# Kernel tuning notes

Measured on AMD Instinct MI355X. Metric: run time of the kernel, lower is better.

## Reference

```python
import jax, jax.numpy as jnp
import numpy as np

B, T, P, D, V = 8, 4096, 4, 512, 256
N = T // P          # 1024 patches (T divisible by P, so no padding needed)
K = 16              # k_retrieval
W = 4               # local message-passing window
H = 8               # refresh attention heads = min(8, D//64)
ROUNDS = 6
EPS = 1e-5


def layer_norm(x, g, b):
    mu = x.mean(-1, keepdims=True)
    var = ((x - mu) ** 2).mean(-1, keepdims=True)
    return (x - mu) / jnp.sqrt(var + EPS) * g + b


def setup_inputs() -> dict:
    key = jax.random.key(0)
    ks = iter(jax.random.split(key, 48))
    w = lambda *s: jax.random.normal(next(ks), s, jnp.float32) * 0.02
    p = {}
    p['x'] = jax.random.randint(next(ks), (B, T), 0, V)
    p['emb'] = w(V, D)
    p['pos_emb'] = w(P, D)
    p['gru_w_ih'] = w(D, 3 * D); p['gru_w_hh'] = w(D, 3 * D)
    p['gru_b_ih'] = jnp.zeros(3 * D); p['gru_b_hh'] = jnp.zeros(3 * D)
    p['patch_ln_g'] = jnp.ones(D); p['patch_ln_b'] = jnp.zeros(D)
    p['summ_w'] = w(D, D); p['summ_b'] = jnp.zeros(D)
    p['msg_w1'] = w(2 * D, D); p['msg_b1'] = jnp.zeros(D)
    p['msg_w2'] = w(D, D); p['msg_b2'] = jnp.zeros(D)
    p['msg_ln_g'] = jnp.ones(D); p['msg_ln_b'] = jnp.zeros(D)
    p['q_w'] = w(D, D); p['q_b'] = jnp.zeros(D)
    p['k_w'] = w(D, D); p['k_b'] = jnp.zeros(D)
    p['v_w'] = w(D, D); p['v_b'] = jnp.zeros(D)
    p['o_w'] = w(D, D); p['o_b'] = jnp.zeros(D)
    p['gc_w_ih'] = w(2 * D, 3 * D); p['gc_w_hh'] = w(D, 3 * D)
    p['gc_b_ih'] = jnp.zeros(3 * D); p['gc_b_hh'] = jnp.zeros(3 * D)
    p['ar_ln_g'] = jnp.ones(D); p['ar_ln_b'] = jnp.zeros(D)
    p['ar_qkv_w'] = w(D, 3 * D); p['ar_qkv_b'] = jnp.zeros(3 * D)
    p['ar_out_w'] = w(D, D); p['ar_out_b'] = jnp.zeros(D)
    p['broad_w'] = w(D, D); p['broad_b'] = jnp.zeros(D)
    p['ln_g'] = jnp.ones(D); p['ln_b'] = jnp.zeros(D)
    p['head_w'] = w(D, V)
    return p


def reference(x, emb, pos_emb, gru_w_ih, gru_w_hh, gru_b_ih, gru_b_hh,
              patch_ln_g, patch_ln_b, summ_w, summ_b,
              msg_w1, msg_b1, msg_w2, msg_b2, msg_ln_g, msg_ln_b,
              q_w, q_b, k_w, k_b, v_w, v_b, o_w, o_b,
              gc_w_ih, gc_w_hh, gc_b_ih, gc_b_hh,
              ar_ln_g, ar_ln_b, ar_qkv_w, ar_qkv_b, ar_out_w, ar_out_b,
              broad_w, broad_b, ln_g, ln_b, head_w):
    # --- patch encoding: embedding + pos + GRU over the P tokens of each patch ---
    flat = x.reshape(B * N, P)
    h = emb[flat] + pos_emb[None, :, :]                      # [B*N, P, D]

    def gru_step(hprev, xt):
        gi = xt @ gru_w_ih + gru_b_ih
        gh = hprev @ gru_w_hh + gru_b_hh
        ir, iz, inn = jnp.split(gi, 3, -1)
        hr, hz, hn = jnp.split(gh, 3, -1)
        r = jax.nn.sigmoid(ir + hr)
        z = jax.nn.sigmoid(iz + hz)
        n = jnp.tanh(inn + r * hn)
        hnew = (1 - z) * n + z * hprev
        return hnew, hnew

    _, hs = jax.lax.scan(gru_step, jnp.zeros((B * N, D), h.dtype), jnp.swapaxes(h, 0, 1))
    local = layer_norm(jnp.swapaxes(hs, 0, 1), patch_ln_g, patch_ln_b).reshape(B, N, P, D)
    h = local.mean(2) @ summ_w + summ_b                      # patch summaries [B, N, D]

    # --- RoPE tables over patch positions ---
    d = D // 2
    inv_freq = 1.0 / (10000.0 ** (jnp.arange(0, D, 2, dtype=jnp.float32) / D))
    freqs = jnp.arange(N, dtype=jnp.float32)[:, None] * inv_freq[None, :]   # [N, d]
    cos, sin = jnp.cos(freqs), jnp.sin(freqs)

    def rotary(t):
        t1, t2 = t[..., :d], t[..., d:]
        return jnp.concatenate([t1 * cos - t2 * sin, t2 * cos + t1 * sin], -1)

    causal = jnp.tril(jnp.ones((N, N), bool))
    hd = D // H

    for rnd in range(ROUNDS):
        # windowed neighbor gather (W past patches + self), fused MLP messages
        padded = jnp.pad(h, ((0, 0), (W, 0), (0, 0)))
        neighbors = jnp.stack([padded[:, W - w:W - w + N] for w in range(W + 1)], 2)  # [B,N,W+1,D]
        self_exp = jnp.broadcast_to(h[:, :, None, :], neighbors.shape)
        msg_in = jnp.concatenate([self_exp, neighbors], -1)
        msgs = (jax.nn.gelu(msg_in @ msg_w1 + msg_b1, approximate=False) @ msg_w2 + msg_b2).mean(2)

        # RoPE top-k sparse causal attention (N > K, sparse branch always taken)
        q = rotary(h @ q_w + q_b)
        k = rotary(h @ k_w + k_b)
        v = h @ v_w + v_b
        scores = jnp.einsum('bnd,bmd->bnm', q, k) / jnp.sqrt(jnp.float32(D))
        scores = jnp.where(causal, scores, -jnp.inf)
        tv, ti = jax.lax.top_k(scores, K)
        probs = jax.nn.softmax(tv, -1)  # == softmax of -inf-filled sparse score matrix
        vg = jax.vmap(lambda vi, ii: vi[ii])(v, ti)          # [B, N, K, D]
        retrieved = jnp.einsum('bnk,bnkd->bnd', probs, vg) @ o_w + o_b

        # GRUCell gated write
        wi = jnp.concatenate([msgs, retrieved], -1)
        gi = wi @ gc_w_ih + gc_b_ih
        gh = h @ gc_w_hh + gc_b_hh
        ir, iz, inn = jnp.split(gi, 3, -1)
        hr, hz, hn = jnp.split(gh, 3, -1)
        r = jax.nn.sigmoid(ir + hr)
        z = jax.nn.sigmoid(iz + hz)
        n = jnp.tanh(inn + r * hn)
        h = layer_norm((1 - z) * n + z * h, msg_ln_g, msg_ln_b)

        # global causal MHA refresh every 2 rounds (eval mode, no dropout)
        if (rnd + 1) % 2 == 0:
            res = h
            hn_ = layer_norm(h, ar_ln_g, ar_ln_b)
            qkv = hn_ @ ar_qkv_w + ar_qkv_b
            qh, kh, vh = [t.reshape(B, N, H, hd) for t in jnp.split(qkv, 3, -1)]
            s = jnp.einsum('bnhd,bmhd->bhnm', qh, kh) / jnp.sqrt(jnp.float32(hd))
            a = jax.nn.softmax(jnp.where(causal, s, -jnp.inf), -1)
            o = jnp.einsum('bhnm,bmhd->bnhd', a, vh).reshape(B, N, D)
            h = res + (o @ ar_out_w + ar_out_b)

    # broadcast patch state back to tokens, project to vocab
    broad = h @ broad_w + broad_b
    final = (local + broad[:, :, None, :]).reshape(B, N * P, D)[:, :T]
    return layer_norm(final, ln_g, ln_b) @ head_w            # [B, T, V]
```

## Files before the change

kernel.cpp:

```cpp
#include <hip/hip_runtime.h>
#include <math.h>

constexpr int CB = 8, CT = 4096, CP = 4, CD = 512, CV = 256;
constexpr int CN = 1024, CK = 16, CH = 8, CHD = 64;
constexpr int ROWS = CB * CN;
constexpr int TROWS = CB * CT;
constexpr float CEPS = 1e-5f;
constexpr size_t PN = (size_t)ROWS * CD;

constexpr size_t OFF_LOCAL = 0;
constexpr size_t OFF_HP    = OFF_LOCAL + (size_t)ROWS * CP * CD;
constexpr size_t OFF_X4    = OFF_HP    + PN;
constexpr size_t OFF_MS    = OFF_X4    + (size_t)ROWS * 2560;
constexpr size_t OFF_A     = OFF_MS    + PN;
constexpr size_t OFF_B     = OFF_A     + PN;
constexpr size_t OFF_BIAS  = OFF_B     + PN;
constexpr size_t OFF_WT    = OFF_BIAS  + 4096;

constexpr size_t TOT_W    = 7471104;
constexpr size_t T_GRU_IH = 0;
constexpr size_t T_GRU_HH = 786432;
constexpr size_t T_SUMM   = 1572864;
constexpr size_t T_FUSE   = 1835008;
constexpr size_t T_MSG2   = 3145728;
constexpr size_t T_OW     = 3407872;
constexpr size_t T_GCAB   = 3670016;
constexpr size_t T_GC_HH  = 5242880;
constexpr size_t T_AR_QKV = 6029312;
constexpr size_t T_AR_OUT = 6815744;
constexpr size_t T_BROAD  = 7077888;
constexpr size_t T_HEAD   = 7340032;

constexpr int F_ACC_F32  = 1;
constexpr int F_ACC_PAIR = 2;
constexpr int F_WR_F32   = 4;
constexpr int F_WR_PAIR  = 8;
constexpr int F_TRI      = 16;
constexpr int F_SPLIT    = 32;

typedef __attribute__((ext_vector_type(8))) short short8;
typedef __attribute__((ext_vector_type(4))) float f32x4;

__device__ __forceinline__ float sigm(float x) { return 1.f / (1.f + expf(-x)); }
__device__ __forceinline__ float geluf(float x) {
  return 0.5f * x * (1.f + erff(x * 0.7071067811865475f));
}
__device__ __forceinline__ unsigned short bf_hi(float x) {
  const unsigned u = __float_as_uint(x);
  return (unsigned short)((u + 0x7FFFu + ((u >> 16) & 1u)) >> 16);
}
__device__ __forceinline__ float bf_f(unsigned short h) {
  return __uint_as_float((unsigned)h << 16);
}
__device__ __forceinline__ void split_store(float v, unsigned short* ph, unsigned short* pl) {
  const unsigned short h = bf_hi(v);
  *ph = h; *pl = bf_hi(v - bf_f(h));
}
__device__ __forceinline__ float blk_sum(float v, float* red) {
#pragma unroll
  for (int o = 32; o > 0; o >>= 1) v += __shfl_down(v, o, 64);
  const int wv = threadIdx.x >> 6, ln = threadIdx.x & 63;
  __syncthreads();
  if (ln == 0) red[wv] = v;
  __syncthreads();
  return red[0] + red[1] + red[2] + red[3];
}

__global__ __launch_bounds__(256) void transpose_split(const float* __restrict__ in,
                                                       unsigned short* __restrict__ oh,
                                                       unsigned short* __restrict__ ol,
                                                       int K, int N, int ldk, int ko)
{
  __shared__ float tile[32][33];
  const int n0 = blockIdx.x * 32, k0 = blockIdx.y * 32;
  const int tx = threadIdx.x & 31, ty = threadIdx.x >> 5;
#pragma unroll
  for (int i = 0; i < 32; i += 8)
    tile[ty + i][tx] = in[(size_t)(k0 + ty + i) * N + n0 + tx];
  __syncthreads();
#pragma unroll
  for (int i = 0; i < 32; i += 8) {
    const float v = tile[tx][ty + i];
    const unsigned short h = bf_hi(v);
    const size_t o = (size_t)(n0 + ty + i) * ldk + ko + k0 + tx;
    oh[o] = h;
    ol[o] = bf_hi(v - bf_f(h));
  }
}

__global__ void concat_bias5(const float* __restrict__ b1, const float* __restrict__ qb,
                             const float* __restrict__ kb, const float* __restrict__ vb,
                             float* __restrict__ o)
{
  const int i = blockIdx.x * 256 + threadIdx.x;
  float v;
  if (i < 512) v = b1[i];
  else if (i < 1024) v = 0.f;
  else if (i < 1536) v = qb[i - 1024];
  else if (i < 2048) v = kb[i - 1536];
  else v = vb[i - 2048];
  o[i] = v;
}

template <bool P3>
__global__ __launch_bounds__(256, 2) void gemm_bf3(
    const unsigned short* __restrict__ AH, const unsigned short* __restrict__ AL,
    const unsigned short* __restrict__ A2H, const unsigned short* __restrict__ A2L,
    int K1, int lda,
    const unsigned short* __restrict__ BH, const unsigned short* __restrict__ BL, int ldb,
    const float* __restrict__ bias, float scale,
    float* __restrict__ Cf, int ldc, float* __restrict__ Cf2,
    unsigned short* __restrict__ CHp, unsigned short* __restrict__ CLp, int ldcp,
    int K, int flags, long long sA, long long sB, long long sC)
{
  AH += (size_t)blockIdx.z * sA; AL += (size_t)blockIdx.z * sA;
  BH += (size_t)blockIdx.z * sB; BL += (size_t)blockIdx.z * sB;
  if (Cf) Cf += (size_t)blockIdx.z * sC;
  int bm, bn;
  if (flags & F_TRI) {
    int t = blockIdx.x, i = 0, acc = 0;
    while (acc + i + 1 <= t) { ++i; acc += i; }
    bm = i << 7; bn = (t - acc) << 7;
  } else {
    bm = blockIdx.y << 7; bn = blockIdx.x << 7;
  }
  __shared__ __align__(16) unsigned short AsH[128][40];
  __shared__ __align__(16) unsigned short AsL[128][40];
  __shared__ __align__(16) unsigned short BsH[128][40];
  __shared__ __align__(16) unsigned short BsL[P3 ? 128 : 1][40];
  const int tid = threadIdx.x;
  const int lane = tid & 63, wave = tid >> 6;
  const int wm = (wave & 1) << 6, wn = (wave >> 1) << 6;
  const int r16 = lane & 15, quad = lane >> 4;
  const int sr = tid >> 1, sc = (tid & 1) << 4;
  const f32x4 zero = {0.f, 0.f, 0.f, 0.f};
  f32x4 acc[4][4];
#pragma unroll
  for (int i = 0; i < 4; ++i)
#pragma unroll
    for (int j = 0; j < 4; ++j) acc[i][j] = zero;

  for (int k0 = 0; k0 < K; k0 += 32) {
    const int kc = k0 + sc;
    const unsigned short *pAH, *pAL;
    if (kc < K1) {
      pAH = AH + (size_t)(bm + sr) * lda + kc;
      pAL = AL + (size_t)(bm + sr) * lda + kc;
    } else {
      pAH = A2H + (size_t)(bm + sr) * lda + (kc - K1);
      pAL = A2L + (size_t)(bm + sr) * lda + (kc - K1);
    }
    const unsigned short* pBH = BH + (size_t)(bn + sr) * ldb + kc;
    *(uint4*)&AsH[sr][sc]     = *(const uint4*)pAH;
    *(uint4*)&AsH[sr][sc + 8] = *(const uint4*)(pAH + 8);
    *(uint4*)&AsL[sr][sc]     = *(const uint4*)pAL;
    *(uint4*)&AsL[sr][sc + 8] = *(const uint4*)(pAL + 8);
    *(uint4*)&BsH[sr][sc]     = *(const uint4*)pBH;
    *(uint4*)&BsH[sr][sc + 8] = *(const uint4*)(pBH + 8);
    if (P3) {
      const unsigned short* pBL = BL + (size_t)(bn + sr) * ldb + kc;
      *(uint4*)&BsL[sr][sc]     = *(const uint4*)pBL;
      *(uint4*)&BsL[sr][sc + 8] = *(const uint4*)(pBL + 8);
    }
    __syncthreads();
    short8 bh[4], bl[4];
#pragma unroll
    for (int ni = 0; ni < 4; ++ni) {
      bh[ni] = *(const short8*)&BsH[wn + ni * 16 + r16][quad * 8];
      if (P3) bl[ni] = *(const short8*)&BsL[wn + ni * 16 + r16][quad * 8];
    }
#pragma unroll
    for (int mi = 0; mi < 4; ++mi) {
      const short8 ah = *(const short8*)&AsH[wm + mi * 16 + r16][quad * 8];
      const short8 al = *(const short8*)&AsL[wm + mi * 16 + r16][quad * 8];
#pragma unroll
      for (int ni = 0; ni < 4; ++ni) {
        acc[mi][ni] = __builtin_amdgcn_mfma_f32_16x16x32_bf16(ah, bh[ni], acc[mi][ni], 0, 0, 0);
        acc[mi][ni] = __builtin_amdgcn_mfma_f32_16x16x32_bf16(al, bh[ni], acc[mi][ni], 0, 0, 0);
        if (P3)
          acc[mi][ni] = __builtin_amdgcn_mfma_f32_16x16x32_bf16(ah, bl[ni], acc[mi][ni], 0, 0, 0);
      }
    }
    __syncthreads();
  }
#pragma unroll
  for (int mi = 0; mi < 4; ++mi) {
    const int row0 = bm + wm + mi * 16 + quad * 4;
#pragma unroll
    for (int ni = 0; ni < 4; ++ni) {
      const int col = bn + wn + ni * 16 + r16;
      const float bv = bias ? bias[col] : 0.f;
#pragma unroll
      for (int rg = 0; rg < 4; ++rg) {
        const int row = row0 + rg;
        float o = acc[mi][ni][rg] * scale + bv;
        if (flags & F_SPLIT) {
          if (col < 1024) {
            float* p = Cf + (size_t)row * ldc + col;
            *p = o + *p;
          } else {
            Cf2[(size_t)row * 512 + (col - 1024)] = o;
          }
        } else {
          if (flags & F_ACC_F32) o += Cf[(size_t)row * ldc + col];
          if (flags & F_ACC_PAIR) {
            const size_t ip = (size_t)row * ldcp + col;
            o += bf_f(CHp[ip]) + bf_f(CLp[ip]);
          }
          if (flags & F_WR_F32) Cf[(size_t)row * ldc + col] = o;
          if (flags & F_WR_PAIR) {
            const size_t ip = (size_t)row * ldcp + col;
            split_store(o, &CHp[ip], &CLp[ip]);
          }
        }
      }
    }
  }
}

__global__ __launch_bounds__(256, 3) void gemm_bf3s(
    const unsigned short* __restrict__ AH, const unsigned short* __restrict__ AL, int lda,
    const unsigned short* __restrict__ BH, int ldb,
    const float* __restrict__ bias,
    float* __restrict__ Cf, int ldc,
    unsigned short* __restrict__ CHp, unsigned short* __restrict__ CLp, int ldcp,
    int K, int flags)
{
  const int bm = blockIdx.y << 6, bn = blockIdx.x << 7;
  __shared__ __align__(16) unsigned short AsH[64][40];
  __shared__ __align__(16) unsigned short AsL[64][40];
  __shared__ __align__(16) unsigned short BsH[128][40];
  const int tid = threadIdx.x;
  const int lane = tid & 63, wave = tid >> 6;
  const int wm = (wave & 1) << 5, wn = (wave >> 1) << 6;
  const int r16 = lane & 15, quad = lane >> 4;
  const int sar = tid >> 2, sac = (tid & 3) << 3;
  const int sbr = tid >> 1, sbc = (tid & 1) << 4;
  const f32x4 zero = {0.f, 0.f, 0.f, 0.f};
  f32x4 acc[2][4];
#pragma unroll
  for (int i = 0; i < 2; ++i)
#pragma unroll
    for (int j = 0; j < 4; ++j) acc[i][j] = zero;

  for (int k0 = 0; k0 < K; k0 += 32) {
    const unsigned short* pAH = AH + (size_t)(bm + sar) * lda + k0 + sac;
    const unsigned short* pAL = AL + (size_t)(bm + sar) * lda + k0 + sac;
    const unsigned short* pBH = BH + (size_t)(bn + sbr) * ldb + k0 + sbc;
    *(uint4*)&AsH[sar][sac] = *(const uint4*)pAH;
    *(uint4*)&AsL[sar][sac] = *(const uint4*)pAL;
    *(uint4*)&BsH[sbr][sbc]     = *(const uint4*)pBH;
    *(uint4*)&BsH[sbr][sbc + 8] = *(const uint4*)(pBH + 8);
    __syncthreads();
    short8 bh[4];
#pragma unroll
    for (int ni = 0; ni < 4; ++ni)
      bh[ni] = *(const short8*)&BsH[wn + ni * 16 + r16][quad * 8];
#pragma unroll
    for (int mi = 0; mi < 2; ++mi) {
      const short8 ah = *(const short8*)&AsH[wm + mi * 16 + r16][quad * 8];
      const short8 al = *(const short8*)&AsL[wm + mi * 16 + r16][quad * 8];
#pragma unroll
      for (int ni = 0; ni < 4; ++ni) {
        acc[mi][ni] = __builtin_amdgcn_mfma_f32_16x16x32_bf16(ah, bh[ni], acc[mi][ni], 0, 0, 0);
        acc[mi][ni] = __builtin_amdgcn_mfma_f32_16x16x32_bf16(al, bh[ni], acc[mi][ni], 0, 0, 0);
      }
    }
    __syncthreads();
  }
#pragma unroll
  for (int mi = 0; mi < 2; ++mi) {
    const int row0 = bm + wm + mi * 16 + quad * 4;
#pragma unroll
    for (int ni = 0; ni < 4; ++ni) {
      const int col = bn + wn + ni * 16 + r16;
      const float bv = bias ? bias[col] : 0.f;
#pragma unroll
      for (int rg = 0; rg < 4; ++rg) {
        const int row = row0 + rg;
        float o = acc[mi][ni][rg] + bv;
        if (flags & F_ACC_PAIR) {
          const size_t ip = (size_t)row * ldcp + col;
          o += bf_f(CHp[ip]) + bf_f(CLp[ip]);
        }
        if (flags & F_WR_F32) Cf[(size_t)row * ldc + col] = o;
        if (flags & F_WR_PAIR) {
          const size_t ip = (size_t)row * ldcp + col;
          split_store(o, &CHp[ip], &CLp[ip]);
        }
      }
    }
  }
}

__global__ void zero_k(float* __restrict__ p) {
  p[(size_t)blockIdx.x * 256 + threadIdx.x] = 0.f;
}

__global__ void embed_p(const int* __restrict__ x, const float* __restrict__ emb,
                        const float* __restrict__ pos,
                        unsigned short* __restrict__ oh, unsigned short* __restrict__ ol, int t)
{
  const int i = blockIdx.x * 256 + threadIdx.x;
  const int r = i >> 9, d = i & 511;
  const int b = r >> 10, n = r & (CN - 1);
  const int tok = x[b * CT + n * CP + t];
  const float v = emb[(size_t)tok * CD + d] + pos[t * CD + d];
  split_store(v, &oh[i], &ol[i]);
}

__global__ void gru_point_p(const float* __restrict__ gi, const float* __restrict__ ghn,
                            unsigned short* __restrict__ hH, unsigned short* __restrict__ hL,
                            float* __restrict__ hs, int t)
{
  const int i = blockIdx.x * 256 + threadIdx.x;
  const int r = i >> 9, d = i & 511;
  const size_t gb = (size_t)r * (3 * CD) + d;
  const float sr_ = gi[gb], sz = gi[gb + CD], inn = gi[gb + 2 * CD];
  const float hn = ghn[i];
  const float hp = bf_f(hH[i]) + bf_f(hL[i]);
  const float rr = sigm(sr_), zz = sigm(sz);
  const float nn = tanhf(inn + rr * hn);
  const float hv = (1.f - zz) * nn + zz * hp;
  split_store(hv, &hH[i], &hL[i]);
  hs[(size_t)r * (CP * CD) + (size_t)t * CD + d] = hv;
}

__global__ __launch_bounds__(256) void ln_rows(const float* __restrict__ in, float* __restrict__ out,
                                               const float* __restrict__ g, const float* __restrict__ b)
{
  const int r = blockIdx.x, t = threadIdx.x;
  __shared__ float red[4];
  const float* ip = in + (size_t)r * CD;
  const float v0 = ip[t], v1 = ip[t + 256];
  const float mu = blk_sum(v0 + v1, red) * (1.f / CD);
  const float d0 = v0 - mu, d1 = v1 - mu;
  const float var = blk_sum(d0 * d0 + d1 * d1, red) * (1.f / CD);
  const float inv = rsqrtf(var + CEPS);
  float* op = out + (size_t)r * CD;
  op[t] = d0 * inv * g[t] + b[t];
  op[t + 256] = d1 * inv * g[t + 256] + b[t + 256];
}

__global__ void mean_pool_p(const float* __restrict__ local,
                            unsigned short* __restrict__ oh, unsigned short* __restrict__ ol)
{
  const int i = blockIdx.x * 256 + threadIdx.x;
  const int r = i >> 9, d = i & 511;
  const float* p = local + (size_t)r * (CP * CD) + d;
  split_store(0.25f * (p[0] + p[CD] + p[2 * CD] + p[3 * CD]), &oh[i], &ol[i]);
}

__global__ void msg_gelu_p(const float* __restrict__ X4,
                           unsigned short* __restrict__ oh, unsigned short* __restrict__ ol)
{
  const int i = blockIdx.x * 256 + threadIdx.x;
  const int r = i >> 9, d = i & 511;
  const int n = r & (CN - 1);
  const float pv = X4[(size_t)r * 2560 + d];
  float acc = 0.f;
#pragma unroll
  for (int w = 0; w <= 4; ++w) {
    const float xv = pv + ((n >= w) ? X4[(size_t)(r - w) * 2560 + 512 + d] : 0.f);
    acc += geluf(xv);
  }
  split_store(acc * 0.2f, &oh[i], &ol[i]);
}

__global__ void rotary2_p(const float* __restrict__ X4,
                          unsigned short* __restrict__ qh, unsigned short* __restrict__ ql,
                          unsigned short* __restrict__ kh, unsigned short* __restrict__ kl)
{
  const int i = blockIdx.x * 256 + threadIdx.x;
  const int r = i >> 8, j = i & 255;
  const int n = r & (CN - 1);
  const float fr = (float)n * expf(-9.210340371976184f * ((float)j * (1.f / 256.f)));
  float s, c;
  sincosf(fr, &s, &c);
  const float* p = X4 + (size_t)r * 2560;
  const size_t o0 = (size_t)r * CD + j, o1 = o0 + 256;
  const float q1 = p[1024 + j], q2 = p[1024 + 256 + j];
  split_store(q1 * c - q2 * s, &qh[o0], &ql[o0]);
  split_store(q2 * c + q1 * s, &qh[o1], &ql[o1]);
  const float k1 = p[1536 + j], k2 = p[1536 + 256 + j];
  split_store(k1 * c - k2 * s, &kh[o0], &kl[o0]);
  split_store(k2 * c + k1 * s, &kh[o1], &kl[o1]);
}

__global__ __launch_bounds__(256) void topk_attn(const float* __restrict__ X4,
                                                 unsigned short* __restrict__ ctxH,
                                                 unsigned short* __restrict__ ctxL)
{
  const int r = blockIdx.x;
  const int b = r >> 10, n = r & (CN - 1);
  const float* row = X4 + (size_t)r * 2560;
  const int tid = threadIdx.x, lane = tid & 63, wave = tid >> 6;
  __shared__ unsigned long long cands[64];
  __shared__ float p16[CK];
  __shared__ int i16[CK];
  unsigned long long key[4];
#pragma unroll
  for (int q = 0; q < 4; ++q) {
    const int m = tid + q * 256;
    const float v = (m <= n) ? row[m] : -INFINITY;
    unsigned u = __float_as_uint(v);
    u = (u & 0x80000000u) ? ~u : (u | 0x80000000u);
    key[q] = ((unsigned long long)u << 32) | (unsigned)(CN - 1 - m);
  }
  unsigned long long mycand = 0ull;
#pragma unroll
  for (int it = 0; it < CK; ++it) {
    unsigned long long best = key[0];
#pragma unroll
    for (int q = 1; q < 4; ++q) best = best > key[q] ? best : key[q];
#pragma unroll
    for (int o = 32; o > 0; o >>= 1) {
      const unsigned long long o2 = __shfl_xor(best, o, 64);
      best = best > o2 ? best : o2;
    }
    if (lane == it) mycand = best;
#pragma unroll
    for (int q = 0; q < 4; ++q)
      if (key[q] == best) key[q] = 0ull;
  }
  if (lane < CK) cands[wave * CK + lane] = mycand;
  __syncthreads();
  if (wave == 0) {
    unsigned long long k2 = cands[lane];
    unsigned long long mine = 0ull;
#pragma unroll
    for (int it = 0; it < CK; ++it) {
      unsigned long long best = k2;
#pragma unroll
      for (int o = 32; o > 0; o >>= 1) {
        const unsigned long long o2 = __shfl_xor(best, o, 64);
        best = best > o2 ? best : o2;
      }
      if (lane == it) mine = best;
      if (k2 == best) k2 = 0ull;
    }
    unsigned u = (unsigned)(mine >> 32);
    u = (u & 0x80000000u) ? (u & 0x7FFFFFFFu) : ~u;
    const float val = __uint_as_float(u);
    const int idx = CN - 1 - (int)(mine & 0xFFFFFFFFu);
    const float mx = __shfl(val, 0, 64);
    float e = 0.f;
    if (lane < CK && val != -INFINITY) e = expf(val - mx);
    float sum = e;
#pragma unroll
    for (int o = 32; o > 0; o >>= 1) sum += __shfl_xor(sum, o, 64);
    if (lane < CK) {
      p16[lane] = e / sum;
      i16[lane] = idx;
    }
  }
  __syncthreads();
  const size_t vb = ((size_t)b << 10);
#pragma unroll
  for (int pass = 0; pass < 2; ++pass) {
    const int d = tid + pass * 256;
    float a = 0.f;
#pragma unroll
    for (int q = 0; q < CK; ++q)
      a += p16[q] * X4[(vb + i16[q]) * 2560 + 2048 + d];
    split_store(a, &ctxH[(size_t)r * CD + d], &ctxL[(size_t)r * CD + d]);
  }
}

__global__ __launch_bounds__(256) void gru_ln_p(const float* __restrict__ gi, const float* __restrict__ ghn,
                                                unsigned short* __restrict__ hH, unsigned short* __restrict__ hL,
                                                const float* __restrict__ g, const float* __restrict__ b,
                                                unsigned short* __restrict__ aH, unsigned short* __restrict__ aL,
                                                const float* __restrict__ g2, const float* __restrict__ b2)
{
  const int r = blockIdx.x, t = threadIdx.x;
  __shared__ float red[4];
  float u[2];
#pragma unroll
  for (int q = 0; q < 2; ++q) {
    const int d = t + q * 256;
    const size_t gb = (size_t)r * (3 * CD) + d;
    const float sr_ = gi[gb], sz = gi[gb + CD], inn = gi[gb + 2 * CD];
    const float hn = ghn[(size_t)r * CD + d];
    const size_t hi = (size_t)r * CD + d;
    const float hp = bf_f(hH[hi]) + bf_f(hL[hi]);
    const float rr = sigm(sr_), zz = sigm(sz);
    const float nn = tanhf(inn + rr * hn);
    u[q] = (1.f - zz) * nn + zz * hp;
  }
  const float mu = blk_sum(u[0] + u[1], red) * (1.f / CD);
  const float d0 = u[0] - mu, d1 = u[1] - mu;
  const float var = blk_sum(d0 * d0 + d1 * d1, red) * (1.f / CD);
  const float inv = rsqrtf(var + CEPS);
  const float h0 = d0 * inv * g[t] + b[t];
  const float h1 = d1 * inv * g[t + 256] + b[t + 256];
  split_store(h0, &hH[(size_t)r * CD + t], &hL[(size_t)r * CD + t]);
  split_store(h1, &hH[(size_t)r * CD + t + 256], &hL[(size_t)r * CD + t + 256]);
  if (aH) {
    const float mu2 = blk_sum(h0 + h1, red) * (1.f / CD);
    const float e0 = h0 - mu2, e1 = h1 - mu2;
    const float var2 = blk_sum(e0 * e0 + e1 * e1, red) * (1.f / CD);
    const float inv2 = rsqrtf(var2 + CEPS);
    split_store(e0 * inv2 * g2[t] + b2[t], &aH[(size_t)r * CD + t], &aL[(size_t)r * CD + t]);
    split_store(e1 * inv2 * g2[t + 256] + b2[t + 256],
                &aH[(size_t)r * CD + t + 256], &aL[(size_t)r * CD + t + 256]);
  }
}

constexpr int FP = 72;
__global__ __launch_bounds__(256, 2) void flash_attn_p(const unsigned short* __restrict__ qkvH,
                                                       const unsigned short* __restrict__ qkvL,
                                                       unsigned short* __restrict__ outH,
                                                       unsigned short* __restrict__ outL)
{
  __shared__ __align__(16) unsigned short Qh[64 * FP], Ql[64 * FP];
  __shared__ __align__(16) unsigned short Kh[64 * FP], Kl[64 * FP];
  __shared__ __align__(16) unsigned short Vth[64 * FP], Vtl[64 * FP];
  __shared__ __align__(16) unsigned short Pm[64 * FP];
  const int qt = blockIdx.x, head = blockIdx.y, b = blockIdx.z;
  const int tid = threadIdx.x;
  const int lane = tid & 63, wave = tid >> 6;
  const int r16 = lane & 15, quad = lane >> 4;
  const size_t base = (size_t)b * CN * (3 * CD) + head * CHD;

  {
    const int r = tid >> 2, c0 = (tid & 3) << 4;
    const unsigned short* qh = qkvH + base + (size_t)(qt * 64 + r) * (3 * CD) + c0;
    const unsigned short* ql = qkvL + base + (size_t)(qt * 64 + r) * (3 * CD) + c0;
    *(uint4*)&Qh[r * FP + c0]     = *(const uint4*)qh;
    *(uint4*)&Qh[r * FP + c0 + 8] = *(const uint4*)(qh + 8);
    *(uint4*)&Ql[r * FP + c0]     = *(const uint4*)ql;
    *(uint4*)&Ql[r * FP + c0 + 8] = *(const uint4*)(ql + 8);
  }
  float m_i[4], l_i[4];
  f32x4 O[4];
  const f32x4 zero = {0.f, 0.f, 0.f, 0.f};
#pragma unroll
  for (int r = 0; r < 4; ++r) { m_i[r] = -INFINITY; l_i[r] = 0.f; }
#pragma unroll
  for (int d = 0; d < 4; ++d) O[d] = zero;

  for (int j = 0; j <= qt; ++j) {
    __syncthreads();
    {
      const int r = tid >> 2, c0 = (tid & 3) << 4;
      const unsigned short* kh = qkvH + base + (size_t)(j * 64 + r) * (3 * CD) + CD + c0;
      const unsigned short* kl = qkvL + base + (size_t)(j * 64 + r) * (3 * CD) + CD + c0;
      *(uint4*)&Kh[r * FP + c0]     = *(const uint4*)kh;
      *(uint4*)&Kh[r * FP + c0 + 8] = *(const uint4*)(kh + 8);
      *(uint4*)&Kl[r * FP + c0]     = *(const uint4*)kl;
      *(uint4*)&Kl[r * FP + c0 + 8] = *(const uint4*)(kl + 8);
      const int rp = (tid >> 3) << 1, c0v = (tid & 7) << 3;
      const unsigned short* v0h = qkvH + base + (size_t)(j * 64 + rp) * (3 * CD) + 2 * CD + c0v;
      const unsigned short* v1h = v0h + 3 * CD;
      const unsigned short* v0l = qkvL + base + (size_t)(j * 64 + rp) * (3 * CD) + 2 * CD + c0v;
      const unsigned short* v1l = v0l + 3 * CD;
      unsigned short xh[8], yh[8], xl[8], yl[8];
      *(uint4*)xh = *(const uint4*)v0h; *(uint4*)yh = *(const uint4*)v1h;
      *(uint4*)xl = *(const uint4*)v0l; *(uint4*)yl = *(const uint4*)v1l;
#pragma unroll
      for (int c = 0; c < 8; ++c) {
        const int R = c0v + c;
        const int col = rp ^ ((R >> 3) << 3);
        *(unsigned*)&Vth[R * FP + col] = (unsigned)xh[c] | ((unsigned)yh[c] << 16);
        *(unsigned*)&Vtl[R * FP + col] = (unsigned)xl[c] | ((unsigned)yl[c] << 16);
      }
    }
    __syncthreads();
    f32x4 S[4];
#pragma unroll
    for (int nt = 0; nt < 4; ++nt) S[nt] = zero;
#pragma unroll
    for (int kh2 = 0; kh2 < 2; ++kh2) {
      const short8 qh = *(const short8*)&Qh[(wave * 16 + r16) * FP + kh2 * 32 + quad * 8];
      const short8 ql = *(const short8*)&Ql[(wave * 16 + r16) * FP + kh2 * 32 + quad * 8];
#pragma unroll
      for (int nt = 0; nt < 4; ++nt) {
        const short8 kkh = *(const short8*)&Kh[(nt * 16 + r16) * FP + kh2 * 32 + quad * 8];
        const short8 kkl = *(const short8*)&Kl[(nt * 16 + r16) * FP + kh2 * 32 + quad * 8];
        S[nt] = __builtin_amdgcn_mfma_f32_16x16x32_bf16(qh, kkh, S[nt], 0, 0, 0);
        S[nt] = __builtin_amdgcn_mfma_f32_16x16x32_bf16(qh, kkl, S[nt], 0, 0, 0);
        S[nt] = __builtin_amdgcn_mfma_f32_16x16x32_bf16(ql, kkh, S[nt], 0, 0, 0);
      }
    }
#pragma unroll
    for (int r = 0; r < 4; ++r) {
      const int qrow = wave * 16 + quad * 4 + r;
      float s[4];
#pragma unroll
      for (int nt = 0; nt < 4; ++nt) {
        s[nt] = S[nt][r] * 0.125f;
        if (j == qt && (nt * 16 + r16) > qrow) s[nt] = -1e30f;
      }
      float rm = fmaxf(fmaxf(s[0], s[1]), fmaxf(s[2], s[3]));
#pragma unroll
      for (int o = 8; o > 0; o >>= 1) rm = fmaxf(rm, __shfl_xor(rm, o, 64));
      const float newm = fmaxf(m_i[r], rm);
      float p[4], rs = 0.f;
#pragma unroll
      for (int nt = 0; nt < 4; ++nt) { p[nt] = expf(s[nt] - newm); rs += p[nt]; }
#pragma unroll
      for (int o = 8; o > 0; o >>= 1) rs += __shfl_xor(rs, o, 64);
      const float alpha = expf(m_i[r] - newm);
      l_i[r] = l_i[r] * alpha + rs;
      m_i[r] = newm;
#pragma unroll
      for (int dt = 0; dt < 4; ++dt) O[dt][r] *= alpha;
#pragma unroll
      for (int nt = 0; nt < 4; ++nt)
        Pm[qrow * FP + nt * 16 + r16] = bf_hi(p[nt]);
    }
    __syncthreads();
#pragma unroll
    for (int kh2 = 0; kh2 < 2; ++kh2) {
      const short8 pa = *(const short8*)&Pm[(wave * 16 + r16) * FP + kh2 * 32 + quad * 8];
#pragma unroll
      for (int dt = 0; dt < 4; ++dt) {
        const int R = dt * 16 + r16;
        const int col = (kh2 * 32 + quad * 8) ^ ((R >> 3) << 3);
        const short8 vh = *(const short8*)&Vth[R * FP + col];
        const short8 vl = *(const short8*)&Vtl[R * FP + col];
        O[dt] = __builtin_amdgcn_mfma_f32_16x16x32_bf16(pa, vh, O[dt], 0, 0, 0);
        O[dt] = __builtin_amdgcn_mfma_f32_16x16x32_bf16(pa, vl, O[dt], 0, 0, 0);
      }
    }
  }
#pragma unroll
  for (int r = 0; r < 4; ++r) {
    const float inv = 1.f / l_i[r];
    const size_t row = (size_t)b * CN + qt * 64 + wave * 16 + quad * 4 + r;
#pragma unroll
    for (int dt = 0; dt < 4; ++dt) {
      const size_t o = row * CD + head * CHD + dt * 16 + r16;
      split_store(O[dt][r] * inv, &outH[o], &outL[o]);
    }
  }
}

__global__ __launch_bounds__(256) void final_ln_p(const float* __restrict__ local,
                                                  const float* __restrict__ broad,
                                                  const float* __restrict__ g, const float* __restrict__ bb,
                                                  unsigned short* __restrict__ oh,
                                                  unsigned short* __restrict__ ol)
{
  const int r = blockIdx.x, t = threadIdx.x;
  __shared__ float red[4];
  const size_t lb = (size_t)r * CD;
  const size_t br = (size_t)(r >> 2) * CD;
  const float v0 = local[lb + t] + broad[br + t];
  const float v1 = local[lb + 256 + t] + broad[br + 256 + t];
  const float mu = blk_sum(v0 + v1, red) * (1.f / CD);
  const float d0 = v0 - mu, d1 = v1 - mu;
  const float var = blk_sum(d0 * d0 + d1 * d1, red) * (1.f / CD);
  const float inv = rsqrtf(var + CEPS);
  split_store(d0 * inv * g[t] + bb[t], &oh[lb + t], &ol[lb + t]);
  split_store(d1 * inv * g[t + 256] + bb[t + 256], &oh[lb + 256 + t], &ol[lb + 256 + t]);
}

extern "C" void kernel_launch(void* const* d_in, const int* in_sizes, int n_in,
                              void* d_out, int out_size, void* d_ws, size_t ws_size,
                              hipStream_t stream)
{
  (void)in_sizes; (void)n_in; (void)out_size; (void)ws_size;
  const int*   x         = (const int*)d_in[0];
  const float* emb       = (const float*)d_in[1];
  const float* pos_emb   = (const float*)d_in[2];
  const float* gru_w_ih  = (const float*)d_in[3];
  const float* gru_w_hh  = (const float*)d_in[4];
  const float* gru_b_ih  = (const float*)d_in[5];
  const float* gru_b_hh  = (const float*)d_in[6];
  const float* patch_g   = (const float*)d_in[7];
  const float* patch_b   = (const float*)d_in[8];
  const float* summ_w    = (const float*)d_in[9];
  const float* summ_b    = (const float*)d_in[10];
  const float* msg_w1    = (const float*)d_in[11];
  const float* msg_b1    = (const float*)d_in[12];
  const float* msg_w2    = (const float*)d_in[13];
  const float* msg_b2    = (const float*)d_in[14];
  const float* msg_ln_g  = (const float*)d_in[15];
  const float* msg_ln_b  = (const float*)d_in[16];
  const float* q_w       = (const float*)d_in[17];
  const float* q_b       = (const float*)d_in[18];
  const float* k_w       = (const float*)d_in[19];
  const float* k_b       = (const float*)d_in[20];
  const float* v_w       = (const float*)d_in[21];
  const float* v_b       = (const float*)d_in[22];
  const float* o_w       = (const float*)d_in[23];
  const float* o_b       = (const float*)d_in[24];
  const float* gc_w_ih   = (const float*)d_in[25];
  const float* gc_w_hh   = (const float*)d_in[26];
  const float* gc_b_ih   = (const float*)d_in[27];
  const float* gc_b_hh   = (const float*)d_in[28];
  const float* ar_ln_g   = (const float*)d_in[29];
  const float* ar_ln_b   = (const float*)d_in[30];
  const float* ar_qkv_w  = (const float*)d_in[31];
  const float* ar_qkv_b  = (const float*)d_in[32];
  const float* ar_out_w  = (const float*)d_in[33];
  const float* ar_out_b  = (const float*)d_in[34];
  const float* broad_w   = (const float*)d_in[35];
  const float* broad_b   = (const float*)d_in[36];
  const float* ln_g      = (const float*)d_in[37];
  const float* ln_b      = (const float*)d_in[38];
  const float* head_w    = (const float*)d_in[39];
  float* out = (float*)d_out;

  float* ws = (float*)d_ws;
  float* WL    = ws + OFF_LOCAL;
  float* X4    = ws + OFF_X4;
  float* GI    = X4;
  float* GHN   = X4 + (size_t)ROWS * 1536;
  float* WBR   = ws + OFF_MS;
  float* Wbias5 = ws + OFF_BIAS;
  unsigned short* WTh = (unsigned short*)(ws + OFF_WT);
  unsigned short* WTl = WTh + TOT_W;
  unsigned short* WhH = (unsigned short*)(ws + OFF_HP);
  unsigned short* WhL = WhH + PN;
  unsigned short* MsH = (unsigned short*)(ws + OFF_MS);
  unsigned short* MsL = MsH + PN;
  unsigned short* pAH = (unsigned short*)(ws + OFF_A);
  unsigned short* pAL = pAH + PN;
  unsigned short* pBH = (unsigned short*)(ws + OFF_B);
  unsigned short* pBL = pBH + PN;
  unsigned short* QkH = (unsigned short*)X4;
  unsigned short* QkL = QkH + (size_t)ROWS * 1536;
  unsigned short* FnH = (unsigned short*)X4;
  unsigned short* FnL = FnH + (size_t)TROWS * CD;

  const int EW = ROWS * CD / 256;
  const float inv_sqrt_d = 0.04419417382415922f;

  auto TR = [&](const float* in, size_t off, int K, int N, int ldk, int ko) {
    transpose_split<<<dim3(N / 32, K / 32), 256, 0, stream>>>(in, WTh + off, WTl + off, K, N, ldk, ko);
  };
  TR(gru_w_ih, T_GRU_IH, 512, 1536, 512, 0);
  TR(gru_w_hh, T_GRU_HH, 512, 1536, 512, 0);
  TR(summ_w,   T_SUMM,   512, 512,  512, 0);
  TR(msg_w1,                      T_FUSE,           512, 512, 512, 0);
  TR(msg_w1 + (size_t)512 * 512,  T_FUSE + 262144,  512, 512, 512, 0);
  TR(q_w,                         T_FUSE + 524288,  512, 512, 512, 0);
  TR(k_w,                         T_FUSE + 786432,  512, 512, 512, 0);
  TR(v_w,                         T_FUSE + 1048576, 512, 512, 512, 0);
  TR(msg_w2,   T_MSG2,   512, 512,  512, 0);
  TR(o_w, T_OW, 512, 512, 512, 0);
  TR(gc_w_ih,                       T_GCAB, 512, 1536, 1024, 0);
  TR(gc_w_ih + (size_t)512 * 1536,  T_GCAB, 512, 1536, 1024, 512);
  TR(gc_w_hh,  T_GC_HH,  512, 1536, 512, 0);
  TR(ar_qkv_w, T_AR_QKV, 512, 1536, 512, 0);
  TR(ar_out_w, T_AR_OUT, 512, 512,  512, 0);
  TR(broad_w,  T_BROAD,  512, 512,  512, 0);
  TR(head_w,   T_HEAD,   512, 256,  512, 0);
  concat_bias5<<<10, 256, 0, stream>>>(msg_b1, q_b, k_b, v_b, Wbias5);

  auto G3 = [&](const unsigned short* AH_, const unsigned short* AL_, int lda_,
                size_t toff, int ldb_, const float* bias_, float* Cf_, int ldc_, float* Cf2_,
                unsigned short* CHp_, unsigned short* CLp_, int ldcp_,
                int K_, int flags_, int gx, int gy) {
    gemm_bf3<false><<<dim3(gx, gy), 256, 0, stream>>>(
        AH_, AL_, AH_, AL_, K_, lda_, WTh + toff, WTl + toff, ldb_, bias_, 1.f,
        Cf_, ldc_, Cf2_, CHp_, CLp_, ldcp_, K_, flags_, 0, 0, 0);
  };
  auto G3S = [&](const unsigned short* AH_, const unsigned short* AL_, int lda_,
                 size_t toff, const float* bias_, float* Cf_, int ldc_,
                 unsigned short* CHp_, unsigned short* CLp_, int ldcp_,
                 int flags_, int gx, int gy) {
    gemm_bf3s<<<dim3(gx, gy), 256, 0, stream>>>(
        AH_, AL_, lda_, WTh + toff, 512, bias_,
        Cf_, ldc_, CHp_, CLp_, ldcp_, 512, flags_);
  };

  zero_k<<<EW, 256, 0, stream>>>(ws + OFF_HP);
  for (int t = 0; t < CP; ++t) {
    embed_p<<<EW, 256, 0, stream>>>(x, emb, pos_emb, pAH, pAL, t);
    G3(pAH, pAL, 512, T_GRU_IH, 512, gru_b_ih, GI, 1536, nullptr,
       nullptr, nullptr, 0, 512, F_WR_F32, 12, 64);
    G3(WhH, WhL, 512, T_GRU_HH, 512, gru_b_hh, GI, 1536, GHN,
       nullptr, nullptr, 0, 512, F_SPLIT, 12, 64);
    gru_point_p<<<EW, 256, 0, stream>>>(GI, GHN, WhH, WhL, WL, t);
  }
  ln_rows<<<TROWS, 256, 0, stream>>>(WL, WL, patch_g, patch_b);
  mean_pool_p<<<EW, 256, 0, stream>>>(WL, pAH, pAL);
  G3S(pAH, pAL, 512, T_SUMM, summ_b, nullptr, 0, WhH, WhL, 512, F_WR_PAIR, 4, 128);

  for (int rnd = 0; rnd < 6; ++rnd) {
    G3(WhH, WhL, 512, T_FUSE, 512, Wbias5, X4, 2560, nullptr,
       nullptr, nullptr, 0, 512, F_WR_F32, 20, 64);
    msg_gelu_p<<<EW, 256, 0, stream>>>(X4, pBH, pBL);
    G3S(pBH, pBL, 512, T_MSG2, msg_b2, nullptr, 0, MsH, MsL, 512, F_WR_PAIR, 4, 128);
    rotary2_p<<<ROWS, 256, 0, stream>>>(X4, pAH, pAL, pBH, pBL);
    gemm_bf3<true><<<dim3(36, 1, CB), 256, 0, stream>>>(
        pAH, pAL, pAH, pAL, 512, 512, pBH, pBL, 512, nullptr, inv_sqrt_d,
        X4, 2560, nullptr, nullptr, nullptr, 0, 512, F_WR_F32 | F_TRI,
        (long long)CN * CD, (long long)CN * CD, (long long)CN * 2560);
    topk_attn<<<ROWS, 256, 0, stream>>>(X4, pAH, pAL);
    G3S(pAH, pAL, 512, T_OW, o_b, nullptr, 0, pBH, pBL, 512, F_WR_PAIR, 4, 128);
    gemm_bf3<false><<<dim3(12, 64), 256, 0, stream>>>(
        MsH, MsL, pBH, pBL, 512, 512, WTh + T_GCAB, WTl + T_GCAB, 1024, gc_b_ih, 1.f,
        GI, 1536, nullptr, nullptr, nullptr, 0, 1024, F_WR_F32, 0, 0, 0);
    G3(WhH, WhL, 512, T_GC_HH, 512, gc_b_hh, GI, 1536, GHN,
       nullptr, nullptr, 0, 512, F_SPLIT, 12, 64);
    if ((rnd & 1) == 1) {
      gru_ln_p<<<ROWS, 256, 0, stream>>>(GI, GHN, WhH, WhL, msg_ln_g, msg_ln_b,
                                         pAH, pAL, ar_ln_g, ar_ln_b);
      G3(pAH, pAL, 512, T_AR_QKV, 512, ar_qkv_b, nullptr, 0, nullptr,
         QkH, QkL, 1536, 512, F_WR_PAIR, 12, 64);
      flash_attn_p<<<dim3(16, CH, CB), 256, 0, stream>>>(QkH, QkL, pBH, pBL);
      G3S(pBH, pBL, 512, T_AR_OUT, ar_out_b, nullptr, 0, WhH, WhL, 512,
          F_ACC_PAIR | F_WR_PAIR, 4, 128);
    } else {
      gru_ln_p<<<ROWS, 256, 0, stream>>>(GI, GHN, WhH, WhL, msg_ln_g, msg_ln_b,
                                         nullptr, nullptr, nullptr, nullptr);
    }
  }

  G3S(WhH, WhL, 512, T_BROAD, broad_b, WBR, 512, nullptr, nullptr, 0, F_WR_F32, 4, 128);
  final_ln_p<<<TROWS, 256, 0, stream>>>(WL, WBR, ln_g, ln_b, FnH, FnL);
  G3S(FnH, FnL, 512, T_HEAD, nullptr, out, CV, nullptr, nullptr, 0, F_WR_F32, 2, 512);
}
```

Before: 4.023 ms.

## Load GEMM tiles directly into LDS and keep attention Q in registers

```diff
diff --git a/kernel.cpp b/kernel.cpp
--- a/kernel.cpp
+++ b/kernel.cpp
@@ -66,6 +66,16 @@
   return red[0] + red[1] + red[2] + red[3];
 }
 
+typedef __attribute__((address_space(1))) const unsigned int* gp1_t;
+typedef __attribute__((address_space(3))) unsigned int* lp3_t;
+__device__ __forceinline__ void gll16(const void* g, void* l) {
+  __builtin_amdgcn_global_load_lds((gp1_t)g, (lp3_t)l, 16, 0, 0);
+}
+
+__device__ __forceinline__ int swz(int row, int quad) {
+  return ((row & ~7) << 5) | (quad << 6) | ((row & 7) << 3);
+}
+
 __global__ __launch_bounds__(256) void transpose_split(const float* __restrict__ in,
                                                        unsigned short* __restrict__ oh,
                                                        unsigned short* __restrict__ ol,
@@ -118,21 +128,22 @@
   if (Cf) Cf += (size_t)blockIdx.z * sC;
   int bm, bn;
   if (flags & F_TRI) {
-    int t = blockIdx.x, i = 0, acc = 0;
-    while (acc + i + 1 <= t) { ++i; acc += i; }
-    bm = i << 7; bn = (t - acc) << 7;
+    int t = blockIdx.x, i = 0, acc0 = 0;
+    while (acc0 + i + 1 <= t) { ++i; acc0 += i; }
+    bm = i << 7; bn = (t - acc0) << 7;
   } else {
     bm = blockIdx.y << 7; bn = blockIdx.x << 7;
   }
-  __shared__ __align__(16) unsigned short AsH[128][40];
-  __shared__ __align__(16) unsigned short AsL[128][40];
-  __shared__ __align__(16) unsigned short BsH[128][40];
-  __shared__ __align__(16) unsigned short BsL[P3 ? 128 : 1][40];
+  __shared__ __align__(16) unsigned short AsH[128 * 32];
+  __shared__ __align__(16) unsigned short AsL[128 * 32];
+  __shared__ __align__(16) unsigned short BsH[128 * 32];
+  __shared__ __align__(16) unsigned short BsL[P3 ? 128 * 32 : 8];
   const int tid = threadIdx.x;
   const int lane = tid & 63, wave = tid >> 6;
   const int wm = (wave & 1) << 6, wn = (wave >> 1) << 6;
   const int r16 = lane & 15, quad = lane >> 4;
-  const int sr = tid >> 1, sc = (tid & 1) << 4;
+  const int lrow = ((lane >> 5) << 3) | (lane & 7);
+  const int lcg8 = ((lane >> 3) & 3) << 3;
   const f32x4 zero = {0.f, 0.f, 0.f, 0.f};
   f32x4 acc[4][4];
 #pragma unroll
@@ -141,38 +152,32 @@
     for (int j = 0; j < 4; ++j) acc[i][j] = zero;
 
   for (int k0 = 0; k0 < K; k0 += 32) {
-    const int kc = k0 + sc;
-    const unsigned short *pAH, *pAL;
-    if (kc < K1) {
-      pAH = AH + (size_t)(bm + sr) * lda + kc;
-      pAL = AL + (size_t)(bm + sr) * lda + kc;
-    } else {
-      pAH = A2H + (size_t)(bm + sr) * lda + (kc - K1);
-      pAL = A2L + (size_t)(bm + sr) * lda + (kc - K1);
-    }
-    const unsigned short* pBH = BH + (size_t)(bn + sr) * ldb + kc;
-    *(uint4*)&AsH[sr][sc]     = *(const uint4*)pAH;
-    *(uint4*)&AsH[sr][sc + 8] = *(const uint4*)(pAH + 8);
-    *(uint4*)&AsL[sr][sc]     = *(const uint4*)pAL;
-    *(uint4*)&AsL[sr][sc + 8] = *(const uint4*)(pAL + 8);
-    *(uint4*)&BsH[sr][sc]     = *(const uint4*)pBH;
-    *(uint4*)&BsH[sr][sc + 8] = *(const uint4*)(pBH + 8);
-    if (P3) {
-      const unsigned short* pBL = BL + (size_t)(bn + sr) * ldb + kc;
-      *(uint4*)&BsL[sr][sc]     = *(const uint4*)pBL;
-      *(uint4*)&BsL[sr][sc + 8] = *(const uint4*)(pBL + 8);
+    const bool p1 = (k0 < K1);
+    const unsigned short* bAH = p1 ? AH : A2H;
+    const unsigned short* bAL = p1 ? AL : A2L;
+    const int ka = (p1 ? k0 : k0 - K1) + lcg8;
+    const int kb = k0 + lcg8;
+#pragma unroll
+    for (int i = 0; i < 2; ++i) {
+      const int chunk = (wave << 1) | i;
+      const size_t ra = (size_t)(bm + (chunk << 4) + lrow) * lda + ka;
+      const size_t rb = (size_t)(bn + (chunk << 4) + lrow) * ldb + kb;
+      gll16(bAH + ra, &AsH[chunk << 9]);
+      gll16(bAL + ra, &AsL[chunk << 9]);
+      gll16(BH + rb, &BsH[chunk << 9]);
+      if (P3) gll16(BL + rb, &BsL[chunk << 9]);
     }
     __syncthreads();
     short8 bh[4], bl[4];
 #pragma unroll
     for (int ni = 0; ni < 4; ++ni) {
-      bh[ni] = *(const short8*)&BsH[wn + ni * 16 + r16][quad * 8];
-      if (P3) bl[ni] = *(const short8*)&BsL[wn + ni * 16 + r16][quad * 8];
+      bh[ni] = *(const short8*)&BsH[swz(wn + ni * 16 + r16, quad)];
+      if (P3) bl[ni] = *(const short8*)&BsL[swz(wn + ni * 16 + r16, quad)];
     }
 #pragma unroll
     for (int mi = 0; mi < 4; ++mi) {
-      const short8 ah = *(const short8*)&AsH[wm + mi * 16 + r16][quad * 8];
-      const short8 al = *(const short8*)&AsL[wm + mi * 16 + r16][quad * 8];
+      const short8 ah = *(const short8*)&AsH[swz(wm + mi * 16 + r16, quad)];
+      const short8 al = *(const short8*)&AsL[swz(wm + mi * 16 + r16, quad)];
 #pragma unroll
       for (int ni = 0; ni < 4; ++ni) {
         acc[mi][ni] = __builtin_amdgcn_mfma_f32_16x16x32_bf16(ah, bh[ni], acc[mi][ni], 0, 0, 0);
@@ -227,15 +232,15 @@
     int K, int flags)
 {
   const int bm = blockIdx.y << 6, bn = blockIdx.x << 7;
-  __shared__ __align__(16) unsigned short AsH[64][40];
-  __shared__ __align__(16) unsigned short AsL[64][40];
-  __shared__ __align__(16) unsigned short BsH[128][40];
+  __shared__ __align__(16) unsigned short AsH[64 * 32];
+  __shared__ __align__(16) unsigned short AsL[64 * 32];
+  __shared__ __align__(16) unsigned short BsH[128 * 32];
   const int tid = threadIdx.x;
   const int lane = tid & 63, wave = tid >> 6;
   const int wm = (wave & 1) << 5, wn = (wave >> 1) << 6;
   const int r16 = lane & 15, quad = lane >> 4;
-  const int sar = tid >> 2, sac = (tid & 3) << 3;
-  const int sbr = tid >> 1, sbc = (tid & 1) << 4;
+  const int lrow = ((lane >> 5) << 3) | (lane & 7);
+  const int lcg8 = ((lane >> 3) & 3) << 3;
   const f32x4 zero = {0.f, 0.f, 0.f, 0.f};
   f32x4 acc[2][4];
 #pragma unroll
@@ -244,22 +249,26 @@
     for (int j = 0; j < 4; ++j) acc[i][j] = zero;
 
   for (int k0 = 0; k0 < K; k0 += 32) {
-    const unsigned short* pAH = AH + (size_t)(bm + sar) * lda + k0 + sac;
-    const unsigned short* pAL = AL + (size_t)(bm + sar) * lda + k0 + sac;
-    const unsigned short* pBH = BH + (size_t)(bn + sbr) * ldb + k0 + sbc;
-    *(uint4*)&AsH[sar][sac] = *(const uint4*)pAH;
-    *(uint4*)&AsL[sar][sac] = *(const uint4*)pAL;
-    *(uint4*)&BsH[sbr][sbc]     = *(const uint4*)pBH;
-    *(uint4*)&BsH[sbr][sbc + 8] = *(const uint4*)(pBH + 8);
+    {
+      const size_t ra = (size_t)(bm + (wave << 4) + lrow) * lda + k0 + lcg8;
+      gll16(AH + ra, &AsH[wave << 9]);
+      gll16(AL + ra, &AsL[wave << 9]);
+#pragma unroll
+      for (int i = 0; i < 2; ++i) {
+        const int chunk = (wave << 1) | i;
+        const size_t rb = (size_t)(bn + (chunk << 4) + lrow) * ldb + k0 + lcg8;
+        gll16(BH + rb, &BsH[chunk << 9]);
+      }
+    }
     __syncthreads();
     short8 bh[4];
 #pragma unroll
     for (int ni = 0; ni < 4; ++ni)
-      bh[ni] = *(const short8*)&BsH[wn + ni * 16 + r16][quad * 8];
+      bh[ni] = *(const short8*)&BsH[swz(wn + ni * 16 + r16, quad)];
 #pragma unroll
     for (int mi = 0; mi < 2; ++mi) {
-      const short8 ah = *(const short8*)&AsH[wm + mi * 16 + r16][quad * 8];
-      const short8 al = *(const short8*)&AsL[wm + mi * 16 + r16][quad * 8];
+      const short8 ah = *(const short8*)&AsH[swz(wm + mi * 16 + r16, quad)];
+      const short8 al = *(const short8*)&AsL[swz(wm + mi * 16 + r16, quad)];
 #pragma unroll
       for (int ni = 0; ni < 4; ++ni) {
         acc[mi][ni] = __builtin_amdgcn_mfma_f32_16x16x32_bf16(ah, bh[ni], acc[mi][ni], 0, 0, 0);
@@ -508,12 +517,11 @@
 }
 
 constexpr int FP = 72;
-__global__ __launch_bounds__(256, 2) void flash_attn_p(const unsigned short* __restrict__ qkvH,
+__global__ __launch_bounds__(256, 3) void flash_attn_p(const unsigned short* __restrict__ qkvH,
                                                        const unsigned short* __restrict__ qkvL,
                                                        unsigned short* __restrict__ outH,
                                                        unsigned short* __restrict__ outL)
 {
-  __shared__ __align__(16) unsigned short Qh[64 * FP], Ql[64 * FP];
   __shared__ __align__(16) unsigned short Kh[64 * FP], Kl[64 * FP];
   __shared__ __align__(16) unsigned short Vth[64 * FP], Vtl[64 * FP];
   __shared__ __align__(16) unsigned short Pm[64 * FP];
@@ -523,14 +531,13 @@
   const int r16 = lane & 15, quad = lane >> 4;
   const size_t base = (size_t)b * CN * (3 * CD) + head * CHD;
 
+  short8 qh_r[2], ql_r[2];
   {
-    const int r = tid >> 2, c0 = (tid & 3) << 4;
-    const unsigned short* qh = qkvH + base + (size_t)(qt * 64 + r) * (3 * CD) + c0;
-    const unsigned short* ql = qkvL + base + (size_t)(qt * 64 + r) * (3 * CD) + c0;
-    *(uint4*)&Qh[r * FP + c0]     = *(const uint4*)qh;
-    *(uint4*)&Qh[r * FP + c0 + 8] = *(const uint4*)(qh + 8);
-    *(uint4*)&Ql[r * FP + c0]     = *(const uint4*)ql;
-    *(uint4*)&Ql[r * FP + c0 + 8] = *(const uint4*)(ql + 8);
+    const size_t qoff = base + (size_t)(qt * 64 + wave * 16 + r16) * (3 * CD) + quad * 8;
+    const unsigned short* qph = qkvH + qoff;
+    const unsigned short* qpl = qkvL + qoff;
+    qh_r[0] = *(const short8*)qph;  qh_r[1] = *(const short8*)(qph + 32);
+    ql_r[0] = *(const short8*)qpl;  ql_r[1] = *(const short8*)(qpl + 32);
   }
   float m_i[4], l_i[4];
   f32x4 O[4];
@@ -572,8 +579,8 @@
     for (int nt = 0; nt < 4; ++nt) S[nt] = zero;
 #pragma unroll
     for (int kh2 = 0; kh2 < 2; ++kh2) {
-      const short8 qh = *(const short8*)&Qh[(wave * 16 + r16) * FP + kh2 * 32 + quad * 8];
-      const short8 ql = *(const short8*)&Ql[(wave * 16 + r16) * FP + kh2 * 32 + quad * 8];
+      const short8 qh = qh_r[kh2];
+      const short8 ql = ql_r[kh2];
 #pragma unroll
       for (int nt = 0; nt < 4; ++nt) {
         const short8 kkh = *(const short8*)&Kh[(nt * 16 + r16) * FP + kh2 * 32 + quad * 8];
```

Result: slower. 4.343 ms (+8.0%).
